# Kernel optimization log

Measured on AMD Instinct MI355X. Metric: run time of the kernel, lower is better.

Reference implementation:

```python
import jax, jax.numpy as jnp
import numpy as np

N_NODES = 50000
N_EDGES = 400000
N_GRAPHS = 512
F = 32        # num_features
NB = 32       # mp_num_basis_fn
ZMAX = 118
CUTOFF = 5.0
NSPH = 9      # (mp_max_degree+1)^2 with max_degree=2
DEG_IDX = jnp.array([0, 1, 1, 1, 2, 2, 2, 2, 2])  # degree of each spherical component


def _bernstein(u, n=NB):
    # reciprocal_bernstein radial basis: Bernstein polynomials of degree n-1 at u in [0,1)
    k = jnp.arange(n, dtype=jnp.float32)
    log_binom = (jax.scipy.special.gammaln(float(n)) - jax.scipy.special.gammaln(k + 1.0)
                 - jax.scipy.special.gammaln(float(n) - k))
    u = jnp.clip(u, 1e-7, 1.0 - 1e-7)[..., None]
    return jnp.exp(log_binom + k * jnp.log(u) + (float(n) - 1.0 - k) * jnp.log1p(-u))


def _smooth_cutoff(r, cutoff=CUTOFF):
    t = r / cutoff
    return jnp.where(t < 1.0, jnp.exp(1.0 - 1.0 / jnp.clip(1.0 - t * t, 1e-7, None)), 0.0)


def _sph(u):
    # real spherical harmonics (cartesian normalization) up to degree 2; u: (E,3) unit vectors
    x, y, z = u[:, 0], u[:, 1], u[:, 2]
    c = jnp.sqrt(jnp.float32(3.0))
    return jnp.stack([jnp.ones_like(x), y, z, x,
                      c * x * y, c * y * z, 0.5 * (3.0 * z * z - 1.0),
                      c * z * x, 0.5 * c * (x * x - y * y)], axis=-1)


def _dense(x, W, b):
    # equivariant Dense: shared kernel over spherical components, bias only on scalar (l=0)
    y = jnp.einsum('nmf,fg->nmg', x, W)
    return y.at[:, 0, :].add(b)


def _silu_gate(x):
    # equivariant silu: scalar channel gates all degrees (scalar part -> exact silu)
    return x * jax.nn.sigmoid(x[:, 0:1, :])


def setup_inputs() -> dict:
    key = jax.random.key(0)
    ks = jax.random.split(key, 24)
    s = 1.0 / np.sqrt(F)
    sb = 1.0 / np.sqrt(NB)
    inp = {
        'positions': 2.0 * jax.random.normal(ks[0], (N_NODES, 3), jnp.float32),
        'embed': jax.random.normal(ks[1], (ZMAX, F), jnp.float32),
        'Wy0': sb * jax.random.normal(ks[2], (3, NB, F), jnp.float32),
        'Wx0': sb * jax.random.normal(ks[3], (3, NB, F), jnp.float32),
        'W1_0': s * jax.random.normal(ks[4], (F, F), jnp.float32),
        'b1_0': jnp.zeros((F,), jnp.float32),
        'W2_0': s * jax.random.normal(ks[5], (F, F), jnp.float32),
        'b2_0': jnp.zeros((F,), jnp.float32),
        'c0': jnp.full((1,), 0.5, jnp.float32),
        'Wr_last': sb * jax.random.normal(ks[6], (NB, F), jnp.float32),
        'W1_1': s * jax.random.normal(ks[7], (F, F), jnp.float32),
        'b1_1': jnp.zeros((F,), jnp.float32),
        'W2_1': s * jax.random.normal(ks[8], (F, F), jnp.float32),
        'b2_1': jnp.zeros((F,), jnp.float32),
        'c1': jnp.full((1,), 0.5, jnp.float32),
        'Wro1': s * jax.random.normal(ks[9], (F, F), jnp.float32),
        'bro1': jnp.zeros((F,), jnp.float32),
        'Wro2': s * jax.random.normal(ks[10], (F, 1), jnp.float32),
        'bro2': jnp.zeros((1,), jnp.float32),
        'atomic_bias': jax.random.normal(ks[11], (ZMAX,), jnp.float32),
        'atomic_numbers': jax.random.randint(ks[12], (N_NODES,), 0, ZMAX, jnp.int32),
        'dst_idx': jax.random.randint(ks[13], (N_EDGES,), 0, N_NODES, jnp.int32),
        'src_idx': jax.random.randint(ks[14], (N_EDGES,), 0, N_NODES, jnp.int32),
        'batch_segments': jnp.sort(jax.random.randint(ks[15], (N_NODES,), 0, N_GRAPHS, jnp.int32)),
        'graph_mask': jnp.ones((N_GRAPHS,), jnp.bool_),
    }
    return inp


def reference(positions, embed, Wy0, Wx0, W1_0, b1_0, W2_0, b2_0, c0,
              Wr_last, W1_1, b1_1, W2_1, b2_1, c1,
              Wro1, bro1, Wro2, bro2, atomic_bias,
              atomic_numbers, dst_idx, src_idx, batch_segments, graph_mask):
    # --- edge geometry (gather_src/gather_dst) ---
    disp = positions[src_idx] - positions[dst_idx]                # (E,3)
    r = jnp.sqrt(jnp.sum(disp * disp, axis=-1) + 1e-12)           # (E,)
    u = disp / r[:, None]
    Y = _sph(u)                                                   # (E,9)
    rbf = _bernstein(r / (r + 1.0)) * _smooth_cutoff(r)[:, None]  # (E,NB)

    # --- atomic embedding, lifted to (N, 9, F) with zero higher degrees ---
    x0 = embed[atomic_numbers]                                    # (N,F)
    x = jnp.concatenate([x0[:, None, :], jnp.zeros((N_NODES, NSPH - 1, F), x0.dtype)], axis=1)

    # --- iteration 0: full-degree equivariant message pass ---
    wy = jnp.einsum('eb,lbf->elf', rbf, Wy0)[:, DEG_IDX, :]       # (E,9,F) radial weights, (0,l)->l path
    wx = jnp.einsum('eb,lbf->elf', rbf, Wx0)[:, DEG_IDX, :]       # (l,0)->l path
    xs = x[src_idx]                                               # (E,9,F)
    msg = wy * Y[:, :, None] * xs[:, 0:1, :] + wx * xs
    y = jax.ops.segment_sum(msg, dst_idx, num_segments=N_NODES)   # (N,9,F)
    y = x + y
    y = _silu_gate(_dense(y, W1_0, b1_0))
    y = _dense(y, W2_0, b2_0)
    x = x + jax.nn.silu(c0) * y                                   # y_nl == 0 (era disabled)

    # --- iteration 1 (last): max_degree=0 message pass, then reduce to scalars ---
    w0 = rbf @ Wr_last                                            # (E,F)
    msg0 = w0 * x[src_idx, 0, :]
    y0 = jax.ops.segment_sum(msg0, dst_idx, num_segments=N_NODES) # (N,F)
    xs0 = x[:, 0, :]                                              # change_max_degree -> scalars
    y0 = xs0 + y0
    y0 = jax.nn.silu(y0 @ W1_1 + b1_1)
    y0 = y0 @ W2_1 + b2_1
    xs0 = xs0 + jax.nn.silu(c1) * y0

    # --- atomic readout and per-graph sum ---
    h = jax.nn.silu(xs0 @ Wro1 + bro1)
    e_atom = (h @ Wro2)[:, 0] + bro2[0] + atomic_bias[atomic_numbers]
    e_graph = jax.ops.segment_sum(e_atom, batch_segments, num_segments=N_GRAPHS)
    return jnp.where(graph_mask, e_graph, 0.0)
```

## Files before the change

kernel.cpp:

```cpp
#include <hip/hip_runtime.h>
#include <math.h>

#define NNODES 50000
#define NEDGES 400000
#define NGRAPHS 512
#define FDIM 32
#define CAP 32

static constexpr float BINOM31[32] = {
    1.f, 31.f, 465.f, 4495.f, 31465.f, 169911.f, 736281.f, 2629575.f,
    7888725.f, 20160075.f, 44352165.f, 84672315.f, 141120525.f, 206253075.f,
    265182525.f, 300540195.f, 300540195.f, 265182525.f, 206253075.f,
    141120525.f, 84672315.f, 44352165.f, 20160075.f, 7888725.f, 2629575.f,
    736281.f, 169911.f, 31465.f, 4495.f, 465.f, 31.f, 1.f
};

__device__ __forceinline__ float fast_rcp(float x) {
    return __builtin_amdgcn_rcpf(x);
}
__device__ __forceinline__ float silu(float x) {
    return x * fast_rcp(1.0f + __expf(-x));
}

__global__ __launch_bounds__(256) void prep(
    const float* __restrict__ pos,
    const float* __restrict__ Wy0, const float* __restrict__ Wx0,
    const float* __restrict__ Wr_last,
    float4* __restrict__ pos4, int* __restrict__ deg,
    float* __restrict__ out,
    float* __restrict__ cwA, float* __restrict__ cwB)
{
    int i = blockIdx.x * 256 + threadIdx.x;
    if (i < NGRAPHS) out[i] = 0.0f;
    if (i < FDIM * FDIM) {
        float b = BINOM31[i >> 5];
        cwA[i] = b * (Wy0[i] + Wx0[i]);
        cwB[i] = b * Wr_last[i];
    }
    if (i < NNODES) {
        pos4[i] = make_float4(pos[3 * i], pos[3 * i + 1], pos[3 * i + 2], 0.f);
        deg[i] = 0;
    }
}

__global__ __launch_bounds__(256) void build_csr(
    const float4* __restrict__ pos4,
    const int* __restrict__ srci, const int* __restrict__ dsti,
    const int* __restrict__ Z,
    float4* __restrict__ pay, int* __restrict__ deg)
{
    int e = blockIdx.x * 256 + threadIdx.x;
    if (e >= NEDGES) return;
    int s = srci[e], d = dsti[e];
    float4 ps = pos4[s];
    float4 pd = pos4[d];
    float dx = ps.x - pd.x, dy = ps.y - pd.y, dz = ps.z - pd.z;
    float r = sqrtf(dx * dx + dy * dy + dz * dz + 1e-12f);
    if (r >= 5.0f) return;

    float t = r * 0.2f;
    float q = fmaxf(1.0f - t * t, 1e-7f);
    float cut = __expf(1.0f - fast_rcp(q));
    float v = fast_rcp(r + 1.0f);
    float v2 = v * v, v4 = v2 * v2, v8 = v4 * v4, v16 = v8 * v8;
    float scale = v16 * v8 * v4 * v2 * v * cut;

    int rank = atomicAdd(&deg[d], 1);
    if (rank < CAP)
        pay[(size_t)d * CAP + rank] =
            make_float4(r, scale, __int_as_float(s), __int_as_float(Z[s]));
}

#define DECLC(CW, K) float C##K = (CW)[(K) * FDIM + f];
#define DECL_ALL_C(CW)                                                      \
    DECLC(CW,0)  DECLC(CW,1)  DECLC(CW,2)  DECLC(CW,3)  DECLC(CW,4)        \
    DECLC(CW,5)  DECLC(CW,6)  DECLC(CW,7)  DECLC(CW,8)  DECLC(CW,9)        \
    DECLC(CW,10) DECLC(CW,11) DECLC(CW,12) DECLC(CW,13) DECLC(CW,14)       \
    DECLC(CW,15) DECLC(CW,16) DECLC(CW,17) DECLC(CW,18) DECLC(CW,19)       \
    DECLC(CW,20) DECLC(CW,21) DECLC(CW,22) DECLC(CW,23) DECLC(CW,24)       \
    DECLC(CW,25) DECLC(CW,26) DECLC(CW,27) DECLC(CW,28) DECLC(CW,29)       \
    DECLC(CW,30) DECLC(CW,31)

#define HEO(KE, KO)                                                        \
    _ea = fmaf(_ea, _r2a, C##KE); _oa = fmaf(_oa, _r2a, C##KO);            \
    _eb = fmaf(_eb, _r2b, C##KE); _ob = fmaf(_ob, _r2b, C##KO);            \
    _ec = fmaf(_ec, _r2c, C##KE); _oc = fmaf(_oc, _r2c, C##KO);            \
    _ed = fmaf(_ed, _r2d, C##KE); _od = fmaf(_od, _r2d, C##KO);

#define GATHER_ACC4(ACC, XSRC, ROWSEL)                                     \
    float ACC = 0.0f;                                                      \
    for (int j = 0; j < dg; j += 4) {                                      \
        int _jm = dg - 1;                                                  \
        int _j1 = min(j + 1, _jm);                                         \
        int _j2 = min(j + 2, _jm);                                         \
        int _j3 = min(j + 3, _jm);                                         \
        float4 _pa = slot[j];    float4 _pb = slot[_j1];                   \
        float4 _pc = slot[_j2];  float4 _pd = slot[_j3];                   \
        float _sa = _pa.y;                                                 \
        float _sb = (j + 1 < dg) ? _pb.y : 0.f;                            \
        float _sc = (j + 2 < dg) ? _pc.y : 0.f;                            \
        float _sd = (j + 3 < dg) ? _pd.y : 0.f;                            \
        float _xa = (XSRC)[(size_t)__float_as_int(_pa.ROWSEL) * FDIM + f]; \
        float _xb = (XSRC)[(size_t)__float_as_int(_pb.ROWSEL) * FDIM + f]; \
        float _xc = (XSRC)[(size_t)__float_as_int(_pc.ROWSEL) * FDIM + f]; \
        float _xd = (XSRC)[(size_t)__float_as_int(_pd.ROWSEL) * FDIM + f]; \
        float _r2a = _pa.x * _pa.x, _r2b = _pb.x * _pb.x;                  \
        float _r2c = _pc.x * _pc.x, _r2d = _pd.x * _pd.x;                  \
        float _ea = C30, _oa = C31, _eb = C30, _ob = C31;                  \
        float _ec = C30, _oc = C31, _ed = C30, _od = C31;                  \
        HEO(28, 29) HEO(26, 27) HEO(24, 25) HEO(22, 23) HEO(20, 21)       \
        HEO(18, 19) HEO(16, 17) HEO(14, 15) HEO(12, 13) HEO(10, 11)       \
        HEO(8, 9)   HEO(6, 7)   HEO(4, 5)   HEO(2, 3)   HEO(0, 1)         \
        float _wa = fmaf(_pa.x, _oa, _ea);                                 \
        float _wb = fmaf(_pb.x, _ob, _eb);                                 \
        float _wc = fmaf(_pc.x, _oc, _ec);                                 \
        float _wd = fmaf(_pd.x, _od, _ed);                                 \
        ACC = fmaf(_sa * _wa, _xa, ACC);                                   \
        ACC = fmaf(_sb * _wb, _xb, ACC);                                   \
        ACC = fmaf(_sc * _wc, _xc, ACC);                                   \
        ACC = fmaf(_sd * _wd, _xd, ACC);                                   \
    }

#define MATVEC32L(RES, WL, YP, BIAS) do {                                  \
    float4 _q0=(YP)[0], _q1=(YP)[1], _q2=(YP)[2], _q3=(YP)[3];             \
    float4 _q4=(YP)[4], _q5=(YP)[5], _q6=(YP)[6], _q7=(YP)[7];             \
    float _a0=(BIAS), _a1=0.f, _a2=0.f, _a3=0.f;                           \
    _a0=fmaf(_q0.x,(WL)[ 0*FDIM+f],_a0); _a0=fmaf(_q0.y,(WL)[ 1*FDIM+f],_a0); \
    _a0=fmaf(_q0.z,(WL)[ 2*FDIM+f],_a0); _a0=fmaf(_q0.w,(WL)[ 3*FDIM+f],_a0); \
    _a1=fmaf(_q1.x,(WL)[ 4*FDIM+f],_a1); _a1=fmaf(_q1.y,(WL)[ 5*FDIM+f],_a1); \
    _a1=fmaf(_q1.z,(WL)[ 6*FDIM+f],_a1); _a1=fmaf(_q1.w,(WL)[ 7*FDIM+f],_a1); \
    _a2=fmaf(_q2.x,(WL)[ 8*FDIM+f],_a2); _a2=fmaf(_q2.y,(WL)[ 9*FDIM+f],_a2); \
    _a2=fmaf(_q2.z,(WL)[10*FDIM+f],_a2); _a2=fmaf(_q2.w,(WL)[11*FDIM+f],_a2); \
    _a3=fmaf(_q3.x,(WL)[12*FDIM+f],_a3); _a3=fmaf(_q3.y,(WL)[13*FDIM+f],_a3); \
    _a3=fmaf(_q3.z,(WL)[14*FDIM+f],_a3); _a3=fmaf(_q3.w,(WL)[15*FDIM+f],_a3); \
    _a0=fmaf(_q4.x,(WL)[16*FDIM+f],_a0); _a0=fmaf(_q4.y,(WL)[17*FDIM+f],_a0); \
    _a0=fmaf(_q4.z,(WL)[18*FDIM+f],_a0); _a0=fmaf(_q4.w,(WL)[19*FDIM+f],_a0); \
    _a1=fmaf(_q5.x,(WL)[20*FDIM+f],_a1); _a1=fmaf(_q5.y,(WL)[21*FDIM+f],_a1); \
    _a1=fmaf(_q5.z,(WL)[22*FDIM+f],_a1); _a1=fmaf(_q5.w,(WL)[23*FDIM+f],_a1); \
    _a2=fmaf(_q6.x,(WL)[24*FDIM+f],_a2); _a2=fmaf(_q6.y,(WL)[25*FDIM+f],_a2); \
    _a2=fmaf(_q6.z,(WL)[26*FDIM+f],_a2); _a2=fmaf(_q6.w,(WL)[27*FDIM+f],_a2); \
    _a3=fmaf(_q7.x,(WL)[28*FDIM+f],_a3); _a3=fmaf(_q7.y,(WL)[29*FDIM+f],_a3); \
    _a3=fmaf(_q7.z,(WL)[30*FDIM+f],_a3); _a3=fmaf(_q7.w,(WL)[31*FDIM+f],_a3); \
    RES = (_a0+_a1)+(_a2+_a3); } while (0)

__global__ __launch_bounds__(256, 4) void fused_a(
    const float4* __restrict__ pay, const int* __restrict__ deg,
    const float* __restrict__ embed, const int* __restrict__ Z,
    const float* __restrict__ cwA,
    const float* __restrict__ W1, const float* __restrict__ b1,
    const float* __restrict__ W2, const float* __restrict__ b2,
    const float* __restrict__ c0,
    float* __restrict__ x1buf)
{
    __shared__ __align__(16) float ylds[4][64];
    __shared__ float W1l[FDIM * FDIM];
    __shared__ float W2l[FDIM * FDIM];
    int tid = threadIdx.x;
    for (int i = tid; i < FDIM * FDIM; i += 256) {
        W1l[i] = W1[i];
        W2l[i] = W2[i];
    }
    __syncthreads();

    int widx = tid >> 6;
    int lane = tid & 63;
    int f    = lane & 31;
    int half = lane >> 5;

    DECL_ALL_C(cwA)

    int n = (blockIdx.x * 4 + widx) * 2 + half;
    const float4* slot = pay + (size_t)n * CAP;
    int dg = min(deg[n], CAP);

    GATHER_ACC4(accv, embed, w)

    float x0 = embed[Z[n] * FDIM + f];
    float yv = x0 + accv;

    float* yrow = &ylds[widx][half * 32];
    const float4* yp = (const float4*)yrow;
    yrow[f] = yv;
    float t;
    MATVEC32L(t, W1l, yp, b1[f]);
    t = silu(t);
    yrow[f] = t;
    float u;
    MATVEC32L(u, W2l, yp, b2[f]);
    x1buf[(size_t)n * FDIM + f] = fmaf(silu(c0[0]), u, x0);
}

__global__ __launch_bounds__(256, 4) void fused_b(
    const float4* __restrict__ pay, const int* __restrict__ deg,
    const float* __restrict__ x1buf, const float* __restrict__ cwB,
    const float* __restrict__ W1, const float* __restrict__ b1,
    const float* __restrict__ W2, const float* __restrict__ b2,
    const float* __restrict__ c1,
    const float* __restrict__ Wro1, const float* __restrict__ bro1,
    const float* __restrict__ Wro2, const float* __restrict__ bro2,
    const float* __restrict__ abias, const int* __restrict__ Z,
    const int* __restrict__ segs,
    float* __restrict__ out)
{
    __shared__ __align__(16) float ylds[4][64];
    __shared__ float W1l[FDIM * FDIM];
    __shared__ float W2l[FDIM * FDIM];
    __shared__ float Wrl[FDIM * FDIM];
    __shared__ float eb[8];
    __shared__ int   sb[8];
    int tid = threadIdx.x;
    for (int i = tid; i < FDIM * FDIM; i += 256) {
        W1l[i] = W1[i];
        W2l[i] = W2[i];
        Wrl[i] = Wro1[i];
    }
    __syncthreads();

    int widx = tid >> 6;
    int lane = tid & 63;
    int f    = lane & 31;
    int half = lane >> 5;

    DECL_ALL_C(cwB)

    int n = (blockIdx.x * 4 + widx) * 2 + half;
    const float4* slot = pay + (size_t)n * CAP;
    int dg = min(deg[n], CAP);

    GATHER_ACC4(accv, x1buf, z)

    float x1 = x1buf[(size_t)n * FDIM + f];
    float yv = x1 + accv;

    float* yrow = &ylds[widx][half * 32];
    const float4* yp = (const float4*)yrow;
    yrow[f] = yv;
    float t;
    MATVEC32L(t, W1l, yp, b1[f]);
    t = silu(t);
    yrow[f] = t;
    float u;
    MATVEC32L(u, W2l, yp, b2[f]);
    float xs0 = fmaf(silu(c1[0]), u, x1);
    yrow[f] = xs0;
    float h;
    MATVEC32L(h, Wrl, yp, bro1[f]);
    float p = silu(h) * Wro2[f];
    p += __shfl_xor(p, 16, 32);
    p += __shfl_xor(p, 8, 32);
    p += __shfl_xor(p, 4, 32);
    p += __shfl_xor(p, 2, 32);
    p += __shfl_xor(p, 1, 32);

    if (f == 0) {
        eb[widx * 2 + half] = p + bro2[0] + abias[Z[n]];
        sb[widx * 2 + half] = segs[n];
    }
    __syncthreads();
    if (tid == 0) {
        float acc = eb[0];
        int cur = sb[0];
        #pragma unroll
        for (int i = 1; i < 8; ++i) {
            if (sb[i] == cur) acc += eb[i];
            else { atomicAdd(&out[cur], acc); cur = sb[i]; acc = eb[i]; }
        }
        atomicAdd(&out[cur], acc);
    }
}

extern "C" void kernel_launch(void* const* d_in, const int* in_sizes, int n_in,
                              void* d_out, int out_size, void* d_ws, size_t ws_size,
                              hipStream_t stream)
{
    const float* pos     = (const float*)d_in[0];
    const float* embed   = (const float*)d_in[1];
    const float* Wy0     = (const float*)d_in[2];
    const float* Wx0     = (const float*)d_in[3];
    const float* W1_0    = (const float*)d_in[4];
    const float* b1_0    = (const float*)d_in[5];
    const float* W2_0    = (const float*)d_in[6];
    const float* b2_0    = (const float*)d_in[7];
    const float* c0      = (const float*)d_in[8];
    const float* Wr_last = (const float*)d_in[9];
    const float* W1_1    = (const float*)d_in[10];
    const float* b1_1    = (const float*)d_in[11];
    const float* W2_1    = (const float*)d_in[12];
    const float* b2_1    = (const float*)d_in[13];
    const float* c1      = (const float*)d_in[14];
    const float* Wro1    = (const float*)d_in[15];
    const float* bro1    = (const float*)d_in[16];
    const float* Wro2    = (const float*)d_in[17];
    const float* bro2    = (const float*)d_in[18];
    const float* abias   = (const float*)d_in[19];
    const int*   Z       = (const int*)d_in[20];
    const int*   dsti    = (const int*)d_in[21];
    const int*   srci    = (const int*)d_in[22];
    const int*   segs    = (const int*)d_in[23];

    float* out = (float*)d_out;

    char* w = (char*)d_ws;
    float4* pay   = (float4*)w;  w += (size_t)NNODES * CAP * 16;
    float*  x1buf = (float*)w;   w += (size_t)NNODES * FDIM * 4;
    float4* pos4  = (float4*)w;  w += (size_t)NNODES * 16;
    int*    deg   = (int*)w;     w += (size_t)NNODES * 4;
    float*  cwA   = (float*)w;   w += FDIM * FDIM * 4;
    float*  cwB   = (float*)w;   w += FDIM * FDIM * 4;

    const int edgeBlocks = (NEDGES + 255) / 256;
    const int nodeBlocks = NNODES / 8;
    const int prepBlocks = (NNODES + 255) / 256;

    prep<<<prepBlocks, 256, 0, stream>>>(pos, Wy0, Wx0, Wr_last,
                                         pos4, deg, out, cwA, cwB);
    build_csr<<<edgeBlocks, 256, 0, stream>>>(pos4, srci, dsti, Z, pay, deg);
    fused_a<<<nodeBlocks, 256, 0, stream>>>(pay, deg, embed, Z, cwA,
                                            W1_0, b1_0, W2_0, b2_0, c0, x1buf);
    fused_b<<<nodeBlocks, 256, 0, stream>>>(pay, deg, x1buf, cwB,
                                            W1_1, b1_1, W2_1, b2_1, c1,
                                            Wro1, bro1, Wro2, bro2,
                                            abias, Z, segs, out);
}
```

Measured before the change: 187.7 us.

## Pad slot lists to multiples of four and software-pipeline payload loads in gathers

Adds a pad_slots kernel that zero-fills each node's slot list up to a multiple of four, so the gather loop no longer needs clamped indices or per-slot masks. It also stores pre-multiplied row offsets in the payload. The gather now prefetches the next four payload entries while computing the current ones, and the first payloads, x0/x1 and coefficients are issued before the shared-weight copy and barrier to hide latency. The cost is an extra kernel launch and extra zero writes. Reading slot[0..3] unconditionally for nodes with zero degree touches unused memory, which is harmless only if that memory is allocated.

Result: no change. 187.4 us (-0.1%).

```diff
diff --git a/kernel.cpp b/kernel.cpp
--- a/kernel.cpp
+++ b/kernel.cpp
@@ -68,7 +68,21 @@
     int rank = atomicAdd(&deg[d], 1);
     if (rank < CAP)
         pay[(size_t)d * CAP + rank] =
-            make_float4(r, scale, __int_as_float(s), __int_as_float(Z[s]));
+            make_float4(r, scale,
+                        __int_as_float(s * FDIM),
+                        __int_as_float(Z[s] * FDIM));
+}
+
+__global__ __launch_bounds__(256) void pad_slots(
+    float4* __restrict__ pay, int* __restrict__ deg)
+{
+    int n = blockIdx.x * 256 + threadIdx.x;
+    if (n >= NNODES) return;
+    int d = min(deg[n], CAP);
+    int dr = (d + 3) & ~3;
+    float4 zf = make_float4(0.f, 0.f, 0.f, 0.f);
+    for (int j = d; j < dr; ++j) pay[(size_t)n * CAP + j] = zf;
+    deg[n] = dr;
 }
 
 #define DECLC(CW, K) float C##K = (CW)[(K) * FDIM + f];
@@ -87,38 +101,39 @@
     _ec = fmaf(_ec, _r2c, C##KE); _oc = fmaf(_oc, _r2c, C##KO);            \
     _ed = fmaf(_ed, _r2d, C##KE); _od = fmaf(_od, _r2d, C##KO);
 
-#define GATHER_ACC4(ACC, XSRC, ROWSEL)                                     \
+#define GATHER_PIPE(ACC, XSRC, ROWSEL)                                     \
     float ACC = 0.0f;                                                      \
-    for (int j = 0; j < dg; j += 4) {                                      \
-        int _jm = dg - 1;                                                  \
-        int _j1 = min(j + 1, _jm);                                         \
-        int _j2 = min(j + 2, _jm);                                         \
-        int _j3 = min(j + 3, _jm);                                         \
-        float4 _pa = slot[j];    float4 _pb = slot[_j1];                   \
-        float4 _pc = slot[_j2];  float4 _pd = slot[_j3];                   \
-        float _sa = _pa.y;                                                 \
-        float _sb = (j + 1 < dg) ? _pb.y : 0.f;                            \
-        float _sc = (j + 2 < dg) ? _pc.y : 0.f;                            \
-        float _sd = (j + 3 < dg) ? _pd.y : 0.f;                            \
-        float _xa = (XSRC)[(size_t)__float_as_int(_pa.ROWSEL) * FDIM + f]; \
-        float _xb = (XSRC)[(size_t)__float_as_int(_pb.ROWSEL) * FDIM + f]; \
-        float _xc = (XSRC)[(size_t)__float_as_int(_pc.ROWSEL) * FDIM + f]; \
-        float _xd = (XSRC)[(size_t)__float_as_int(_pd.ROWSEL) * FDIM + f]; \
-        float _r2a = _pa.x * _pa.x, _r2b = _pb.x * _pb.x;                  \
-        float _r2c = _pc.x * _pc.x, _r2d = _pd.x * _pd.x;                  \
-        float _ea = C30, _oa = C31, _eb = C30, _ob = C31;                  \
-        float _ec = C30, _oc = C31, _ed = C30, _od = C31;                  \
-        HEO(28, 29) HEO(26, 27) HEO(24, 25) HEO(22, 23) HEO(20, 21)       \
-        HEO(18, 19) HEO(16, 17) HEO(14, 15) HEO(12, 13) HEO(10, 11)       \
-        HEO(8, 9)   HEO(6, 7)   HEO(4, 5)   HEO(2, 3)   HEO(0, 1)         \
-        float _wa = fmaf(_pa.x, _oa, _ea);                                 \
-        float _wb = fmaf(_pb.x, _ob, _eb);                                 \
-        float _wc = fmaf(_pc.x, _oc, _ec);                                 \
-        float _wd = fmaf(_pd.x, _od, _ed);                                 \
-        ACC = fmaf(_sa * _wa, _xa, ACC);                                   \
-        ACC = fmaf(_sb * _wb, _xb, ACC);                                   \
-        ACC = fmaf(_sc * _wc, _xc, ACC);                                   \
-        ACC = fmaf(_sd * _wd, _xd, ACC);                                   \
+    if (dgr > 0) {                                                         \
+        float4 _pa = _h0, _pb = _h1, _pc = _h2, _pd = _h3;                 \
+        for (int j = 0; ; j += 4) {                                        \
+            float _xa = (XSRC)[__float_as_int(_pa.ROWSEL) + f];            \
+            float _xb = (XSRC)[__float_as_int(_pb.ROWSEL) + f];            \
+            float _xc = (XSRC)[__float_as_int(_pc.ROWSEL) + f];            \
+            float _xd = (XSRC)[__float_as_int(_pd.ROWSEL) + f];            \
+            bool _more = (j + 4) < dgr;                                    \
+            float4 _na, _nb, _nc, _nd;                                     \
+            if (_more) {                                                   \
+                _na = slot[j + 4]; _nb = slot[j + 5];                      \
+                _nc = slot[j + 6]; _nd = slot[j + 7];                      \
+            }                                                              \
+            float _r2a = _pa.x * _pa.x, _r2b = _pb.x * _pb.x;              \
+            float _r2c = _pc.x * _pc.x, _r2d = _pd.x * _pd.x;              \
+            float _ea = C30, _oa = C31, _eb = C30, _ob = C31;              \
+            float _ec = C30, _oc = C31, _ed = C30, _od = C31;              \
+            HEO(28, 29) HEO(26, 27) HEO(24, 25) HEO(22, 23) HEO(20, 21)   \
+            HEO(18, 19) HEO(16, 17) HEO(14, 15) HEO(12, 13) HEO(10, 11)   \
+            HEO(8, 9)   HEO(6, 7)   HEO(4, 5)   HEO(2, 3)   HEO(0, 1)     \
+            float _wa = fmaf(_pa.x, _oa, _ea);                             \
+            float _wb = fmaf(_pb.x, _ob, _eb);                             \
+            float _wc = fmaf(_pc.x, _oc, _ec);                             \
+            float _wd = fmaf(_pd.x, _od, _ed);                             \
+            ACC = fmaf(_pa.y * _wa, _xa, ACC);                             \
+            ACC = fmaf(_pb.y * _wb, _xb, ACC);                             \
+            ACC = fmaf(_pc.y * _wc, _xc, ACC);                             \
+            ACC = fmaf(_pd.y * _wd, _xd, ACC);                             \
+            if (!_more) break;                                             \
+            _pa = _na; _pb = _nb; _pc = _nc; _pd = _nd;                    \
+        }                                                                  \
     }
 
 #define MATVEC32L(RES, WL, YP, BIAS) do {                                  \
@@ -156,26 +171,27 @@
     __shared__ float W1l[FDIM * FDIM];
     __shared__ float W2l[FDIM * FDIM];
     int tid = threadIdx.x;
-    for (int i = tid; i < FDIM * FDIM; i += 256) {
-        W1l[i] = W1[i];
-        W2l[i] = W2[i];
-    }
-    __syncthreads();
-
     int widx = tid >> 6;
     int lane = tid & 63;
     int f    = lane & 31;
     int half = lane >> 5;
 
-    DECL_ALL_C(cwA)
-
     int n = (blockIdx.x * 4 + widx) * 2 + half;
     const float4* slot = pay + (size_t)n * CAP;
-    int dg = min(deg[n], CAP);
-
-    GATHER_ACC4(accv, embed, w)
-
+    int dgr = deg[n];
+    float4 _h0 = slot[0], _h1 = slot[1];
+    float4 _h2 = slot[2], _h3 = slot[3];
     float x0 = embed[Z[n] * FDIM + f];
+    DECL_ALL_C(cwA)
+
+    for (int i = tid; i < FDIM * FDIM; i += 256) {
+        W1l[i] = W1[i];
+        W2l[i] = W2[i];
+    }
+    __syncthreads();
+
+    GATHER_PIPE(accv, embed, w)
+
     float yv = x0 + accv;
 
     float* yrow = &ylds[widx][half * 32];
@@ -209,6 +225,20 @@
     __shared__ float eb[8];
     __shared__ int   sb[8];
     int tid = threadIdx.x;
+    int widx = tid >> 6;
+    int lane = tid & 63;
+    int f    = lane & 31;
+    int half = lane >> 5;
+
+    int n = (blockIdx.x * 4 + widx) * 2 + half;
+    const float4* slot = pay + (size_t)n * CAP;
+    int dgr = deg[n];
+    float4 _h0 = slot[0], _h1 = slot[1];
+    float4 _h2 = slot[2], _h3 = slot[3];
+    float x1 = x1buf[(size_t)n * FDIM + f];
+    int   zn = Z[n];
+    DECL_ALL_C(cwB)
+
     for (int i = tid; i < FDIM * FDIM; i += 256) {
         W1l[i] = W1[i];
         W2l[i] = W2[i];
@@ -216,20 +246,8 @@
     }
     __syncthreads();
 
-    int widx = tid >> 6;
-    int lane = tid & 63;
-    int f    = lane & 31;
-    int half = lane >> 5;
-
-    DECL_ALL_C(cwB)
-
-    int n = (blockIdx.x * 4 + widx) * 2 + half;
-    const float4* slot = pay + (size_t)n * CAP;
-    int dg = min(deg[n], CAP);
-
-    GATHER_ACC4(accv, x1buf, z)
-
-    float x1 = x1buf[(size_t)n * FDIM + f];
+    GATHER_PIPE(accv, x1buf, z)
+
     float yv = x1 + accv;
 
     float* yrow = &ylds[widx][half * 32];
@@ -253,7 +271,7 @@
     p += __shfl_xor(p, 1, 32);
 
     if (f == 0) {
-        eb[widx * 2 + half] = p + bro2[0] + abias[Z[n]];
+        eb[widx * 2 + half] = p + bro2[0] + abias[zn];
         sb[widx * 2 + half] = segs[n];
     }
     __syncthreads();
@@ -315,6 +333,7 @@
     prep<<<prepBlocks, 256, 0, stream>>>(pos, Wy0, Wx0, Wr_last,
                                          pos4, deg, out, cwA, cwB);
     build_csr<<<edgeBlocks, 256, 0, stream>>>(pos4, srci, dsti, Z, pay, deg);
+    pad_slots<<<prepBlocks, 256, 0, stream>>>(pay, deg);
     fused_a<<<nodeBlocks, 256, 0, stream>>>(pay, deg, embed, Z, cwA,
                                             W1_0, b1_0, W2_0, b2_0, c0, x1buf);
     fused_b<<<nodeBlocks, 256, 0, stream>>>(pay, deg, x1buf, cwB,
```
